# Optimization experiments

Hardware: AMD Instinct MI355X
Metric: run time of the kernel (lower is better)

The kernel has to match this reference:

```python
import jax, jax.numpy as jnp
import numpy as np

B, N, E, F, OUT = 2, 50000, 150000, 256, 256

def setup_inputs() -> dict:
    key = jax.random.key(0)
    ks = jax.random.split(key, 8)
    X = jax.random.normal(ks[0], (B, N, F), dtype=jnp.float32)
    e = jax.random.uniform(ks[1], (B, E), dtype=jnp.float32)
    ri_idx = jax.random.randint(ks[2], (B, E), 0, N, dtype=jnp.int32)
    ro_idx = jax.random.randint(ks[3], (B, E), 0, N, dtype=jnp.int32)
    W1 = jax.random.normal(ks[4], (3 * F, OUT), dtype=jnp.float32) * (1.0 / np.sqrt(3 * F))
    b1 = jnp.zeros((OUT,), dtype=jnp.float32)
    W2 = jax.random.normal(ks[5], (OUT, OUT), dtype=jnp.float32) * (1.0 / np.sqrt(OUT))
    b2 = jnp.zeros((OUT,), dtype=jnp.float32)
    return {"X": X, "e": e, "ri_idx": ri_idx, "ro_idx": ro_idx,
            "W1": W1, "b1": b1, "W2": W2, "b2": b2}


def _aggregate(x, ew, ri, ro):
    # x: [N,F], ew: [E], ri/ro: [E] receiver/sender node ids per edge.
    # bi = Ri^T X = x[ri]; bo = Ro^T X = x[ro]
    # mi = Ri diag(e) bo : scatter-add weighted sender feats to receivers
    # mo = Ro diag(e) bi : scatter-add weighted receiver feats to senders
    n = x.shape[0]
    w = ew[:, None]
    mi = jax.ops.segment_sum(w * x[ro], ri, num_segments=n)
    mo = jax.ops.segment_sum(w * x[ri], ro, num_segments=n)
    return mi, mo


def reference(X, e, ri_idx, ro_idx, W1, b1, W2, b2):
    mi, mo = jax.vmap(_aggregate)(X, e, ri_idx, ro_idx)   # each [B,N,F]
    M = jnp.concatenate([mi, mo, X], axis=2)              # [B,N,3F]
    h = jnp.tanh(M @ W1 + b1)
    return jnp.tanh(h @ W2 + b2)
```

## Files before the change

### kernel.cpp

```cpp
#include <hip/hip_runtime.h>
#include <hip/hip_bf16.h>
#include <cstdint>
#include <cstddef>

#define BATCH 2
#define NNODE 50000
#define NEDGE 150000
#define FDIM 256
#define MTOT (BATCH * NNODE)
#define NSEG (2 * BATCH * NNODE)
#define SCAN_NB 98

typedef __attribute__((ext_vector_type(8))) __bf16 bf16x8;
typedef __attribute__((ext_vector_type(8))) ushort u16x8;
typedef __attribute__((ext_vector_type(4))) float f32x4;
typedef __attribute__((ext_vector_type(4))) uint32_t u32x4;

typedef const __attribute__((address_space(1))) uint32_t* gptr_t;
typedef __attribute__((address_space(3))) uint32_t* lptr_t;

__device__ __forceinline__ ushort f32_to_bf16_rne(float x) {
    uint32_t u = __builtin_bit_cast(uint32_t, x);
    u = (u + 0x7fffu + ((u >> 16) & 1u)) >> 16;
    return (ushort)u;
}

__device__ __forceinline__ void split2(float x, ushort& h, ushort& l) {
    h = f32_to_bf16_rne(x);
    float hf = __builtin_bit_cast(float, ((uint32_t)h) << 16);
    l = f32_to_bf16_rne(x - hf);
}

__global__ __launch_bounds__(256)
void prep_kernel(const float* __restrict__ W1, const float* __restrict__ W2,
                 ushort* __restrict__ i1h, ushort* __restrict__ i1l,
                 ushort* __restrict__ i2h, ushort* __restrict__ i2l) {
    int idx = blockIdx.x * 256 + threadIdx.x;
    if (idx < 24576) {
        int kb = idx >> 10;
        int col = (idx >> 2) & 255;
        int s = idx & 3;
        int cb = col >> 7, c = col & 127;
        int sw = s ^ ((c >> 1) & 3);
        ushort hs[8], ls[8];
#pragma unroll
        for (int j = 0; j < 8; ++j) {
            int k = kb * 32 + sw * 8 + j;
            split2(W1[(size_t)k * 256 + col], hs[j], ls[j]);
        }
        size_t off = ((size_t)(kb * 2 + cb) * 128 + c) * 32 + s * 8;
#pragma unroll
        for (int j = 0; j < 8; ++j) { i1h[off + j] = hs[j]; i1l[off + j] = ls[j]; }
    }
    if (idx < 8192) {
        int kb = idx >> 10;
        int col = (idx >> 2) & 255;
        int s = idx & 3;
        int cb = col >> 7, c = col & 127;
        int sw = s ^ ((c >> 1) & 3);
        ushort hs[8], ls[8];
#pragma unroll
        for (int j = 0; j < 8; ++j) {
            int k = kb * 32 + sw * 8 + j;
            split2(W2[(size_t)k * 256 + col], hs[j], ls[j]);
        }
        size_t off = ((size_t)(kb * 2 + cb) * 128 + c) * 32 + s * 8;
#pragma unroll
        for (int j = 0; j < 8; ++j) { i2h[off + j] = hs[j]; i2l[off + j] = ls[j]; }
    }
}

__global__ __launch_bounds__(256)
void hist_kernel(const int* __restrict__ ri, const int* __restrict__ ro,
                 int* __restrict__ cnt) {
    int j = blockIdx.x * 256 + threadIdx.x;
    if (j >= BATCH * NEDGE) return;
    int b = j / NEDGE;
    atomicAdd(&cnt[(0 * BATCH + b) * NNODE + ri[j]], 1);
    atomicAdd(&cnt[(1 * BATCH + b) * NNODE + ro[j]], 1);
}

__global__ __launch_bounds__(256)
void scan1_kernel(const int* __restrict__ cnt, int* __restrict__ rs,
                  int* __restrict__ bsum) {
    __shared__ int s[256];
    int tid = threadIdx.x;
    int base = blockIdx.x * 2048 + tid * 8;
    int v[8];
    int loc = 0;
#pragma unroll
    for (int j = 0; j < 8; ++j) {
        int idx = base + j;
        int x = (idx < NSEG) ? cnt[idx] : 0;
        v[j] = x;
        loc += x;
    }
    s[tid] = loc;
    __syncthreads();
    for (int off = 1; off < 256; off <<= 1) {
        int t = (tid >= off) ? s[tid - off] : 0;
        __syncthreads();
        s[tid] += t;
        __syncthreads();
    }
    int run = (tid == 0) ? 0 : s[tid - 1];
#pragma unroll
    for (int j = 0; j < 8; ++j) {
        int idx = base + j;
        if (idx < NSEG) rs[idx] = run;
        run += v[j];
    }
    if (tid == 255) bsum[blockIdx.x] = s[255];
}

__global__ __launch_bounds__(128)
void scan2_kernel(int* __restrict__ bsum) {
    __shared__ int s[128];
    int tid = threadIdx.x;
    int x = (tid < SCAN_NB) ? bsum[tid] : 0;
    s[tid] = x;
    __syncthreads();
    for (int off = 1; off < 128; off <<= 1) {
        int t = (tid >= off) ? s[tid - off] : 0;
        __syncthreads();
        s[tid] += t;
        __syncthreads();
    }
    int ex = (tid == 0) ? 0 : s[tid - 1];
    if (tid < SCAN_NB) bsum[tid] = ex;
}

__global__ __launch_bounds__(256)
void scan3_kernel(int* __restrict__ rs, int* __restrict__ cur,
                  const int* __restrict__ bsum) {
    int base = blockIdx.x * 2048 + threadIdx.x * 8;
    int off = bsum[blockIdx.x];
#pragma unroll
    for (int j = 0; j < 8; ++j) {
        int idx = base + j;
        if (idx < NSEG) {
            int v = rs[idx] + off;
            rs[idx] = v;
            cur[idx] = v;
        }
    }
}

__global__ __launch_bounds__(256)
void fill_kernel(const int* __restrict__ ri, const int* __restrict__ ro,
                 const float* __restrict__ e, int* __restrict__ cur,
                 int* __restrict__ pidx, float* __restrict__ pw) {
    int j = blockIdx.x * 256 + threadIdx.x;
    if (j >= BATCH * NEDGE) return;
    int b = j / NEDGE;
    int vri = ri[j], vro = ro[j];
    float ew = e[j];
    int p0 = atomicAdd(&cur[(0 * BATCH + b) * NNODE + vri], 1);
    pidx[p0] = vro;
    pw[p0] = ew;
    int p1 = atomicAdd(&cur[(1 * BATCH + b) * NNODE + vro], 1);
    pidx[p1] = vri;
    pw[p1] = ew;
}

__global__ __launch_bounds__(256)
void gather_kernel(const float* __restrict__ X, const int* __restrict__ rs,
                   const int* __restrict__ cnt, const int* __restrict__ pidx,
                   const float* __restrict__ pw,
                   float* __restrict__ mi, float* __restrict__ mo) {
    int gid = blockIdx.x * 256 + threadIdx.x;
    int w = gid >> 6;
    int lane = gid & 63;
    if (w >= NSEG) return;
    int t = w / (BATCH * NNODE);
    int r = w - t * (BATCH * NNODE);
    int b = r / NNODE;
    int start = rs[w];
    int c = cnt[w];
    int end = start + c;
    const float* Xb = X + (size_t)b * NNODE * FDIM + lane * 4;
    float4 acc = make_float4(0.f, 0.f, 0.f, 0.f);
    int i = start;
    for (; i + 1 < end; i += 2) {
        int v0 = pidx[i], v1 = pidx[i + 1];
        float w0 = pw[i], w1 = pw[i + 1];
        float4 x0 = *(const float4*)(Xb + (size_t)v0 * FDIM);
        float4 x1 = *(const float4*)(Xb + (size_t)v1 * FDIM);
        acc.x += w0 * x0.x + w1 * x1.x;
        acc.y += w0 * x0.y + w1 * x1.y;
        acc.z += w0 * x0.z + w1 * x1.z;
        acc.w += w0 * x0.w + w1 * x1.w;
    }
    if (i < end) {
        int v0 = pidx[i];
        float w0 = pw[i];
        float4 x0 = *(const float4*)(Xb + (size_t)v0 * FDIM);
        acc.x += w0 * x0.x;
        acc.y += w0 * x0.y;
        acc.z += w0 * x0.z;
        acc.w += w0 * x0.w;
    }
    float* dst = (t == 0 ? mi : mo) + (size_t)r * FDIM + lane * 4;
    *(float4*)dst = acc;
}

template<int NT, int AMODE>
__global__ __launch_bounds__(256, 2)
void gemm_kernel(const float* __restrict__ A0, const float* __restrict__ A1,
                 const float* __restrict__ A2,
                 const ushort* __restrict__ Bh_img, const ushort* __restrict__ Bl_img,
                 const float* __restrict__ bias,
                 uint32_t* __restrict__ hout, float* __restrict__ fout) {
    __shared__ char smem[65536];

    int tid = threadIdx.x;
    int lane = tid & 63;
    int w = tid >> 6;
    int wm = w >> 1, wn = w & 1;
    int r0 = blockIdx.x * 128;
    int cb = blockIdx.y;
    int c0 = cb * 128;

    f32x4 acc[4][4];
    f32x4 zero4 = {0.f, 0.f, 0.f, 0.f};
#pragma unroll
    for (int m = 0; m < 4; ++m)
#pragma unroll
        for (int n = 0; n < 4; ++n) acc[m][n] = zero4;

    auto stage = [&](int buf, int t) {
        const char* asrc;
        int kb;
        if constexpr (AMODE == 0) {
            if (t < 8)       { asrc = (const char*)A0; kb = t * 128; }
            else if (t < 16) { asrc = (const char*)A1; kb = (t - 8) * 128; }
            else             { asrc = (const char*)A2; kb = (t - 16) * 128; }
        } else {
            asrc = (const char*)A0; kb = t * 128;
        }
        char* abase = smem + buf * 16384;
#pragma unroll
        for (int i = 0; i < 4; ++i) {
            int inst = w * 4 + i;
            int row = inst * 8 + (lane >> 3);
            int rowg = r0 + row;
            if (rowg > MTOT - 1) rowg = MTOT - 1;
            int slot = (lane & 7) ^ (row & 7);
            const char* g = asrc + (size_t)rowg * 1024 + kb + slot * 16;
            __builtin_amdgcn_global_load_lds((gptr_t)g, (lptr_t)(abase + inst * 1024), 16, 0, 0);
        }
        int blk = t * 2 + cb;
        const ushort* sh = Bh_img + (size_t)blk * 4096;
        const ushort* sl = Bl_img + (size_t)blk * 4096;
        char* bhbase = smem + 32768 + buf * 16384;
        char* blbase = bhbase + 8192;
#pragma unroll
        for (int j = 0; j < 2; ++j) {
            int inst = w * 2 + j;
            __builtin_amdgcn_global_load_lds((gptr_t)(sh + inst * 512 + lane * 8),
                                             (lptr_t)(bhbase + inst * 1024), 16, 0, 0);
            __builtin_amdgcn_global_load_lds((gptr_t)(sl + inst * 512 + lane * 8),
                                             (lptr_t)(blbase + inst * 1024), 16, 0, 0);
        }
    };

    stage(0, 0);
    asm volatile("s_waitcnt vmcnt(0)" ::: "memory");
    __builtin_amdgcn_s_barrier();

    int cur = 0;
    for (int t = 0; t < NT; ++t) {
        if (t + 1 < NT) stage(cur ^ 1, t + 1);

        char* abase = smem + cur * 16384;
        char* bhbase = smem + 32768 + cur * 16384;
        char* blbase = bhbase + 8192;

        bf16x8 ah[4], al[4], bh[4], bl[4];
        int q0 = (lane >> 4) * 2;
#pragma unroll
        for (int m = 0; m < 4; ++m) {
            int row = wm * 64 + m * 16 + (lane & 15);
            const char* rp = abase + row * 128;
            if constexpr (AMODE == 0) {
                f32x4 lo = *(const f32x4*)(rp + ((q0) ^ (row & 7)) * 16);
                f32x4 hi = *(const f32x4*)(rp + ((q0 + 1) ^ (row & 7)) * 16);
                float v[8] = {lo[0], lo[1], lo[2], lo[3], hi[0], hi[1], hi[2], hi[3]};
                u16x8 hv, lv;
#pragma unroll
                for (int j = 0; j < 8; ++j) {
                    ushort hh, ll;
                    split2(v[j], hh, ll);
                    hv[j] = hh;
                    lv[j] = ll;
                }
                ah[m] = __builtin_bit_cast(bf16x8, hv);
                al[m] = __builtin_bit_cast(bf16x8, lv);
            } else {
                u32x4 lo = *(const u32x4*)(rp + ((q0) ^ (row & 7)) * 16);
                u32x4 hi = *(const u32x4*)(rp + ((q0 + 1) ^ (row & 7)) * 16);
                u16x8 hv, lv;
#pragma unroll
                for (int j = 0; j < 4; ++j) {
                    hv[j] = (ushort)lo[j];
                    lv[j] = (ushort)(lo[j] >> 16);
                    hv[j + 4] = (ushort)hi[j];
                    lv[j + 4] = (ushort)(hi[j] >> 16);
                }
                ah[m] = __builtin_bit_cast(bf16x8, hv);
                al[m] = __builtin_bit_cast(bf16x8, lv);
            }
        }
        int ks = lane >> 4;
#pragma unroll
        for (int n = 0; n < 4; ++n) {
            int c = wn * 64 + n * 16 + (lane & 15);
            int so = (ks ^ ((c >> 1) & 3)) * 16;
            bh[n] = *(const bf16x8*)(bhbase + c * 64 + so);
            bl[n] = *(const bf16x8*)(blbase + c * 64 + so);
        }
#pragma unroll
        for (int m = 0; m < 4; ++m)
#pragma unroll
            for (int n = 0; n < 4; ++n) {
                acc[m][n] = __builtin_amdgcn_mfma_f32_16x16x32_bf16(ah[m], bh[n], acc[m][n], 0, 0, 0);
                acc[m][n] = __builtin_amdgcn_mfma_f32_16x16x32_bf16(al[m], bh[n], acc[m][n], 0, 0, 0);
                acc[m][n] = __builtin_amdgcn_mfma_f32_16x16x32_bf16(ah[m], bl[n], acc[m][n], 0, 0, 0);
            }

        asm volatile("s_waitcnt vmcnt(0)" ::: "memory");
        __builtin_amdgcn_s_barrier();
        cur ^= 1;
    }

#pragma unroll
    for (int m = 0; m < 4; ++m) {
        int rbase = r0 + wm * 64 + m * 16 + ((lane >> 4) * 4);
#pragma unroll
        for (int n = 0; n < 4; ++n) {
            int col = c0 + wn * 64 + n * 16 + (lane & 15);
            float bv = bias[col];
#pragma unroll
            for (int q = 0; q < 4; ++q) {
                int row = rbase + q;
                if (row < MTOT) {
                    float tv = tanhf(acc[m][n][q] + bv);
                    if constexpr (AMODE == 0) {
                        ushort h, l;
                        split2(tv, h, l);
                        hout[(size_t)row * 256 + col] = (uint32_t)h | ((uint32_t)l << 16);
                    } else {
                        fout[(size_t)row * 256 + col] = tv;
                    }
                }
            }
        }
    }
}

extern "C" void kernel_launch(void* const* d_in, const int* in_sizes, int n_in,
                              void* d_out, int out_size, void* d_ws, size_t ws_size,
                              hipStream_t stream) {
    const float* X  = (const float*)d_in[0];
    const float* e  = (const float*)d_in[1];
    const int*   ri = (const int*)d_in[2];
    const int*   ro = (const int*)d_in[3];
    const float* W1 = (const float*)d_in[4];
    const float* b1 = (const float*)d_in[5];
    const float* W2 = (const float*)d_in[6];
    const float* b2 = (const float*)d_in[7];
    float* out = (float*)d_out;

    char* ws = (char*)d_ws;
    const size_t szMI = (size_t)MTOT * 256 * 4;
    float*    mi   = (float*)ws;
    float*    mo   = (float*)(ws + szMI);
    char*     hreg = ws + 2 * szMI;
    uint32_t* hbuf = (uint32_t*)hreg;
    ushort*   i1h  = (ushort*)(ws + 3 * szMI);
    ushort*   i1l  = i1h + 196608;
    ushort*   i2h  = i1l + 196608;
    ushort*   i2l  = i2h + 65536;

    int*   cnt  = (int*)(hreg);
    int*   rs   = (int*)(hreg + 800000);
    int*   cur  = (int*)(hreg + 1600000);
    int*   bsum = (int*)(hreg + 2400000);
    int*   pidx = (int*)(hreg + 2404096);
    float* pw   = (float*)(hreg + 4804096);

    hipMemsetAsync(cnt, 0, (size_t)NSEG * 4, stream);

    prep_kernel<<<96, 256, 0, stream>>>(W1, W2, i1h, i1l, i2h, i2l);

    hist_kernel<<<(BATCH * NEDGE + 255) / 256, 256, 0, stream>>>(ri, ro, cnt);
    scan1_kernel<<<SCAN_NB, 256, 0, stream>>>(cnt, rs, bsum);
    scan2_kernel<<<1, 128, 0, stream>>>(bsum);
    scan3_kernel<<<SCAN_NB, 256, 0, stream>>>(rs, cur, bsum);
    fill_kernel<<<(BATCH * NEDGE + 255) / 256, 256, 0, stream>>>(ri, ro, e, cur, pidx, pw);

    gather_kernel<<<NSEG / 4, 256, 0, stream>>>(X, rs, cnt, pidx, pw, mi, mo);

    dim3 grid1((MTOT + 127) / 128, 2);
    gemm_kernel<24, 0><<<grid1, 256, 0, stream>>>(
        mi, mo, X, i1h, i1l, b1, hbuf, nullptr);

    gemm_kernel<8, 1><<<grid1, 256, 0, stream>>>(
        (const float*)hbuf, nullptr, nullptr, i2h, i2l, b2, nullptr, out);
}
```

Measured before the change: 676.3 us.

## Pre-split aggregates and X into bf16 hi/lo planes; pad edge lists to four

The gather kernel now writes mi/mo as separate bf16 hi and lo planes instead of fp32. When workspace allows, X is also pre-split by a new kernel. The first GEMM then loads A tiles already split, which removes the per-tile float-to-bf16x2 conversion from its inner loop. Edge lists per segment are padded to multiples of four, with the padding zero-filled by a larger memset, so the gather can use vector int4/float4 index and weight loads. This costs an extra pass over X and more workspace, and the extra memset covers the padded edge arrays.

```diff
diff --git a/kernel.cpp b/kernel.cpp
--- a/kernel.cpp
+++ b/kernel.cpp
@@ -71,6 +71,18 @@
 }
 
 __global__ __launch_bounds__(256)
+void xsplit_kernel(const float* __restrict__ X,
+                   ushort* __restrict__ Xh, ushort* __restrict__ Xl) {
+    size_t i = (size_t)blockIdx.x * 256 + threadIdx.x;
+    float4 v = *(const float4*)(X + i * 4);
+    ushort h0, l0, h1, l1, h2, l2, h3, l3;
+    split2(v.x, h0, l0); split2(v.y, h1, l1);
+    split2(v.z, h2, l2); split2(v.w, h3, l3);
+    *(ushort4*)(Xh + i * 4) = make_ushort4(h0, h1, h2, h3);
+    *(ushort4*)(Xl + i * 4) = make_ushort4(l0, l1, l2, l3);
+}
+
+__global__ __launch_bounds__(256)
 void hist_kernel(const int* __restrict__ ri, const int* __restrict__ ro,
                  int* __restrict__ cnt) {
     int j = blockIdx.x * 256 + threadIdx.x;
@@ -92,6 +104,7 @@
     for (int j = 0; j < 8; ++j) {
         int idx = base + j;
         int x = (idx < NSEG) ? cnt[idx] : 0;
+        x = (x + 3) & ~3;
         v[j] = x;
         loc += x;
     }
@@ -167,7 +180,8 @@
 void gather_kernel(const float* __restrict__ X, const int* __restrict__ rs,
                    const int* __restrict__ cnt, const int* __restrict__ pidx,
                    const float* __restrict__ pw,
-                   float* __restrict__ mi, float* __restrict__ mo) {
+                   ushort* __restrict__ mih, ushort* __restrict__ mil,
+                   ushort* __restrict__ moh, ushort* __restrict__ mol) {
     int gid = blockIdx.x * 256 + threadIdx.x;
     int w = gid >> 6;
     int lane = gid & 63;
@@ -176,38 +190,37 @@
     int r = w - t * (BATCH * NNODE);
     int b = r / NNODE;
     int start = rs[w];
-    int c = cnt[w];
-    int end = start + c;
+    int c4 = (cnt[w] + 3) & ~3;
     const float* Xb = X + (size_t)b * NNODE * FDIM + lane * 4;
     float4 acc = make_float4(0.f, 0.f, 0.f, 0.f);
-    int i = start;
-    for (; i + 1 < end; i += 2) {
-        int v0 = pidx[i], v1 = pidx[i + 1];
-        float w0 = pw[i], w1 = pw[i + 1];
-        float4 x0 = *(const float4*)(Xb + (size_t)v0 * FDIM);
-        float4 x1 = *(const float4*)(Xb + (size_t)v1 * FDIM);
-        acc.x += w0 * x0.x + w1 * x1.x;
-        acc.y += w0 * x0.y + w1 * x1.y;
-        acc.z += w0 * x0.z + w1 * x1.z;
-        acc.w += w0 * x0.w + w1 * x1.w;
-    }
-    if (i < end) {
-        int v0 = pidx[i];
-        float w0 = pw[i];
-        float4 x0 = *(const float4*)(Xb + (size_t)v0 * FDIM);
-        acc.x += w0 * x0.x;
-        acc.y += w0 * x0.y;
-        acc.z += w0 * x0.z;
-        acc.w += w0 * x0.w;
-    }
-    float* dst = (t == 0 ? mi : mo) + (size_t)r * FDIM + lane * 4;
-    *(float4*)dst = acc;
-}
-
-template<int NT, int AMODE>
+    for (int i = 0; i < c4; i += 4) {
+        int4 v = *(const int4*)(pidx + start + i);
+        float4 wv = *(const float4*)(pw + start + i);
+        float4 x0 = *(const float4*)(Xb + (size_t)v.x * FDIM);
+        float4 x1 = *(const float4*)(Xb + (size_t)v.y * FDIM);
+        float4 x2 = *(const float4*)(Xb + (size_t)v.z * FDIM);
+        float4 x3 = *(const float4*)(Xb + (size_t)v.w * FDIM);
+        acc.x += wv.x * x0.x + wv.y * x1.x + wv.z * x2.x + wv.w * x3.x;
+        acc.y += wv.x * x0.y + wv.y * x1.y + wv.z * x2.y + wv.w * x3.y;
+        acc.z += wv.x * x0.z + wv.y * x1.z + wv.z * x2.z + wv.w * x3.z;
+        acc.w += wv.x * x0.w + wv.y * x1.w + wv.z * x2.w + wv.w * x3.w;
+    }
+    ushort h0, l0, h1, l1, h2, l2, h3, l3;
+    split2(acc.x, h0, l0); split2(acc.y, h1, l1);
+    split2(acc.z, h2, l2); split2(acc.w, h3, l3);
+    size_t o = (size_t)r * FDIM + lane * 4;
+    ushort* ph = (t == 0 ? mih : moh);
+    ushort* pl = (t == 0 ? mil : mol);
+    *(ushort4*)(ph + o) = make_ushort4(h0, h1, h2, h3);
+    *(ushort4*)(pl + o) = make_ushort4(l0, l1, l2, l3);
+}
+
+template<int NT, int AMODE, bool XPL>
 __global__ __launch_bounds__(256, 2)
-void gemm_kernel(const float* __restrict__ A0, const float* __restrict__ A1,
-                 const float* __restrict__ A2,
+void gemm_kernel(const ushort* __restrict__ Ah0, const ushort* __restrict__ Al0,
+                 const ushort* __restrict__ Ah1, const ushort* __restrict__ Al1,
+                 const ushort* __restrict__ Axh, const ushort* __restrict__ Axl,
+                 const float* __restrict__ Xf,
                  const ushort* __restrict__ Bh_img, const ushort* __restrict__ Bl_img,
                  const float* __restrict__ bias,
                  uint32_t* __restrict__ hout, float* __restrict__ fout) {
@@ -229,25 +242,52 @@
         for (int n = 0; n < 4; ++n) acc[m][n] = zero4;
 
     auto stage = [&](int buf, int t) {
-        const char* asrc;
-        int kb;
+        char* abase = smem + buf * 16384;
         if constexpr (AMODE == 0) {
-            if (t < 8)       { asrc = (const char*)A0; kb = t * 128; }
-            else if (t < 16) { asrc = (const char*)A1; kb = (t - 8) * 128; }
-            else             { asrc = (const char*)A2; kb = (t - 16) * 128; }
+            if (XPL || t < 16) {
+                const ushort *hp, *lp;
+                int kb;
+                if (t < 8)       { hp = Ah0; lp = Al0; kb = t * 32; }
+                else if (t < 16) { hp = Ah1; lp = Al1; kb = (t - 8) * 32; }
+                else             { hp = Axh; lp = Axl; kb = (t - 16) * 32; }
+#pragma unroll
+                for (int i = 0; i < 2; ++i) {
+                    int j = w * 2 + i;
+                    int ks = j & 3, half = j >> 2;
+                    int rowg = r0 + half * 64 + lane;
+                    if (rowg > MTOT - 1) rowg = MTOT - 1;
+                    size_t go = (size_t)rowg * 512 + (size_t)(kb + ks * 8) * 2;
+                    int ld = (ks * 128 + half * 64) * 16;
+                    __builtin_amdgcn_global_load_lds((gptr_t)((const char*)hp + go),
+                                                     (lptr_t)(abase + ld), 16, 0, 0);
+                    __builtin_amdgcn_global_load_lds((gptr_t)((const char*)lp + go),
+                                                     (lptr_t)(abase + 8192 + ld), 16, 0, 0);
+                }
+            } else {
+                int kb = (t - 16) * 128;
+#pragma unroll
+                for (int i = 0; i < 4; ++i) {
+                    int inst = w * 4 + i;
+                    int row = inst * 8 + (lane >> 3);
+                    int rowg = r0 + row;
+                    if (rowg > MTOT - 1) rowg = MTOT - 1;
+                    int slot = (lane & 7) ^ (row & 7);
+                    const char* g = (const char*)Xf + (size_t)rowg * 1024 + kb + slot * 16;
+                    __builtin_amdgcn_global_load_lds((gptr_t)g, (lptr_t)(abase + inst * 1024), 16, 0, 0);
+                }
+            }
         } else {
-            asrc = (const char*)A0; kb = t * 128;
-        }
-        char* abase = smem + buf * 16384;
-#pragma unroll
-        for (int i = 0; i < 4; ++i) {
-            int inst = w * 4 + i;
-            int row = inst * 8 + (lane >> 3);
-            int rowg = r0 + row;
-            if (rowg > MTOT - 1) rowg = MTOT - 1;
-            int slot = (lane & 7) ^ (row & 7);
-            const char* g = asrc + (size_t)rowg * 1024 + kb + slot * 16;
-            __builtin_amdgcn_global_load_lds((gptr_t)g, (lptr_t)(abase + inst * 1024), 16, 0, 0);
+            int kb = t * 128;
+#pragma unroll
+            for (int i = 0; i < 4; ++i) {
+                int inst = w * 4 + i;
+                int row = inst * 8 + (lane >> 3);
+                int rowg = r0 + row;
+                if (rowg > MTOT - 1) rowg = MTOT - 1;
+                int slot = (lane & 7) ^ (row & 7);
+                const char* g = (const char*)Ah0 + (size_t)rowg * 1024 + kb + slot * 16;
+                __builtin_amdgcn_global_load_lds((gptr_t)g, (lptr_t)(abase + inst * 1024), 16, 0, 0);
+            }
         }
         int blk = t * 2 + cb;
         const ushort* sh = Bh_img + (size_t)blk * 4096;
@@ -277,41 +317,50 @@
         char* blbase = bhbase + 8192;
 
         bf16x8 ah[4], al[4], bh[4], bl[4];
-        int q0 = (lane >> 4) * 2;
-#pragma unroll
-        for (int m = 0; m < 4; ++m) {
-            int row = wm * 64 + m * 16 + (lane & 15);
-            const char* rp = abase + row * 128;
-            if constexpr (AMODE == 0) {
-                f32x4 lo = *(const f32x4*)(rp + ((q0) ^ (row & 7)) * 16);
-                f32x4 hi = *(const f32x4*)(rp + ((q0 + 1) ^ (row & 7)) * 16);
-                float v[8] = {lo[0], lo[1], lo[2], lo[3], hi[0], hi[1], hi[2], hi[3]};
-                u16x8 hv, lv;
-#pragma unroll
-                for (int j = 0; j < 8; ++j) {
-                    ushort hh, ll;
-                    split2(v[j], hh, ll);
-                    hv[j] = hh;
-                    lv[j] = ll;
+        int ks = lane >> 4;
+        if (AMODE == 0 && (XPL || t < 16)) {
+#pragma unroll
+            for (int m = 0; m < 4; ++m) {
+                int rowf = wm * 64 + m * 16 + (lane & 15);
+                ah[m] = *(const bf16x8*)(abase + (ks * 128 + rowf) * 16);
+                al[m] = *(const bf16x8*)(abase + 8192 + (ks * 128 + rowf) * 16);
+            }
+        } else {
+            int q0 = ks * 2;
+#pragma unroll
+            for (int m = 0; m < 4; ++m) {
+                int row = wm * 64 + m * 16 + (lane & 15);
+                const char* rp = abase + row * 128;
+                if constexpr (AMODE == 0) {
+                    f32x4 lo = *(const f32x4*)(rp + ((q0) ^ (row & 7)) * 16);
+                    f32x4 hi = *(const f32x4*)(rp + ((q0 + 1) ^ (row & 7)) * 16);
+                    float v[8] = {lo[0], lo[1], lo[2], lo[3], hi[0], hi[1], hi[2], hi[3]};
+                    u16x8 hv, lv;
+#pragma unroll
+                    for (int j = 0; j < 8; ++j) {
+                        ushort hh, ll;
+                        split2(v[j], hh, ll);
+                        hv[j] = hh;
+                        lv[j] = ll;
+                    }
+                    ah[m] = __builtin_bit_cast(bf16x8, hv);
+                    al[m] = __builtin_bit_cast(bf16x8, lv);
+                } else {
+                    u32x4 lo = *(const u32x4*)(rp + ((q0) ^ (row & 7)) * 16);
+                    u32x4 hi = *(const u32x4*)(rp + ((q0 + 1) ^ (row & 7)) * 16);
+                    u16x8 hv, lv;
+#pragma unroll
+                    for (int j = 0; j < 4; ++j) {
+                        hv[j] = (ushort)lo[j];
+                        lv[j] = (ushort)(lo[j] >> 16);
+                        hv[j + 4] = (ushort)hi[j];
+                        lv[j + 4] = (ushort)(hi[j] >> 16);
+                    }
+                    ah[m] = __builtin_bit_cast(bf16x8, hv);
+                    al[m] = __builtin_bit_cast(bf16x8, lv);
                 }
-                ah[m] = __builtin_bit_cast(bf16x8, hv);
-                al[m] = __builtin_bit_cast(bf16x8, lv);
-            } else {
-                u32x4 lo = *(const u32x4*)(rp + ((q0) ^ (row & 7)) * 16);
-                u32x4 hi = *(const u32x4*)(rp + ((q0 + 1) ^ (row & 7)) * 16);
-                u16x8 hv, lv;
-#pragma unroll
-                for (int j = 0; j < 4; ++j) {
-                    hv[j] = (ushort)lo[j];
-                    lv[j] = (ushort)(lo[j] >> 16);
-                    hv[j + 4] = (ushort)hi[j];
-                    lv[j + 4] = (ushort)(hi[j] >> 16);
-                }
-                ah[m] = __builtin_bit_cast(bf16x8, hv);
-                al[m] = __builtin_bit_cast(bf16x8, lv);
-            }
-        }
-        int ks = lane >> 4;
+            }
+        }
 #pragma unroll
         for (int n = 0; n < 4; ++n) {
             int c = wn * 64 + n * 16 + (lane & 15);
@@ -372,39 +421,54 @@
     float* out = (float*)d_out;
 
     char* ws = (char*)d_ws;
-    const size_t szMI = (size_t)MTOT * 256 * 4;
-    float*    mi   = (float*)ws;
-    float*    mo   = (float*)(ws + szMI);
-    char*     hreg = ws + 2 * szMI;
+    const size_t szP = (size_t)MTOT * 256 * 2;
+    ushort* mih = (ushort*)ws;
+    ushort* mil = (ushort*)(ws + szP);
+    ushort* moh = (ushort*)(ws + 2 * szP);
+    ushort* mol = (ushort*)(ws + 3 * szP);
+    char*   hreg = ws + 4 * szP;
     uint32_t* hbuf = (uint32_t*)hreg;
-    ushort*   i1h  = (ushort*)(ws + 3 * szMI);
-    ushort*   i1l  = i1h + 196608;
-    ushort*   i2h  = i1l + 196608;
-    ushort*   i2l  = i2h + 65536;
+    char*   img = hreg + 2 * szP;
+    ushort* i1h = (ushort*)img;
+    ushort* i1l = i1h + 196608;
+    ushort* i2h = i1l + 196608;
+    ushort* i2l = i2h + 65536;
+    char*   xw  = img + 1048576;
+    ushort* Xh  = (ushort*)xw;
+    ushort* Xl  = (ushort*)(xw + szP);
+    const size_t NEED_XPL = 4 * szP + 2 * szP + 1048576 + 2 * szP;
+    bool xpl = ws_size >= NEED_XPL;
 
     int*   cnt  = (int*)(hreg);
     int*   rs   = (int*)(hreg + 800000);
-    int*   cur  = (int*)(hreg + 1600000);
+    int*   curp = (int*)(hreg + 1600000);
     int*   bsum = (int*)(hreg + 2400000);
     int*   pidx = (int*)(hreg + 2404096);
-    float* pw   = (float*)(hreg + 4804096);
-
-    hipMemsetAsync(cnt, 0, (size_t)NSEG * 4, stream);
+    float* pw   = (float*)(hreg + 7204096);
+
+    hipMemsetAsync(hreg, 0, 12004096, stream);
 
     prep_kernel<<<96, 256, 0, stream>>>(W1, W2, i1h, i1l, i2h, i2l);
+    if (xpl) xsplit_kernel<<<25000, 256, 0, stream>>>(X, Xh, Xl);
 
     hist_kernel<<<(BATCH * NEDGE + 255) / 256, 256, 0, stream>>>(ri, ro, cnt);
     scan1_kernel<<<SCAN_NB, 256, 0, stream>>>(cnt, rs, bsum);
     scan2_kernel<<<1, 128, 0, stream>>>(bsum);
-    scan3_kernel<<<SCAN_NB, 256, 0, stream>>>(rs, cur, bsum);
-    fill_kernel<<<(BATCH * NEDGE + 255) / 256, 256, 0, stream>>>(ri, ro, e, cur, pidx, pw);
-
-    gather_kernel<<<NSEG / 4, 256, 0, stream>>>(X, rs, cnt, pidx, pw, mi, mo);
+    scan3_kernel<<<SCAN_NB, 256, 0, stream>>>(rs, curp, bsum);
+    fill_kernel<<<(BATCH * NEDGE + 255) / 256, 256, 0, stream>>>(ri, ro, e, curp, pidx, pw);
+
+    gather_kernel<<<NSEG / 4, 256, 0, stream>>>(X, rs, cnt, pidx, pw, mih, mil, moh, mol);
 
     dim3 grid1((MTOT + 127) / 128, 2);
-    gemm_kernel<24, 0><<<grid1, 256, 0, stream>>>(
-        mi, mo, X, i1h, i1l, b1, hbuf, nullptr);
-
-    gemm_kernel<8, 1><<<grid1, 256, 0, stream>>>(
-        (const float*)hbuf, nullptr, nullptr, i2h, i2l, b2, nullptr, out);
-}
+    if (xpl) {
+        gemm_kernel<24, 0, true><<<grid1, 256, 0, stream>>>(
+            mih, mil, moh, mol, Xh, Xl, X, i1h, i1l, b1, hbuf, nullptr);
+    } else {
+        gemm_kernel<24, 0, false><<<grid1, 256, 0, stream>>>(
+            mih, mil, moh, mol, nullptr, nullptr, X, i1h, i1l, b1, hbuf, nullptr);
+    }
+
+    gemm_kernel<8, 1, false><<<grid1, 256, 0, stream>>>(
+        (const ushort*)hbuf, nullptr, nullptr, nullptr, nullptr, nullptr, nullptr,
+        i2h, i2l, b2, nullptr, out);
+}
```

Result: slower. 716.6 us (+6.0%).
